# Performance work log

Hardware: AMD Instinct MI355X
Metric: run time of the kernel (lower is better)

## Reference

```python
import jax, jax.numpy as jnp
import numpy as np

N, D, DFF, E, F, K, H = 4096, 512, 512, 512, 4096, 1024, 4


def _rn(i, shape, s=0.02):
    return jax.random.normal(jax.random.fold_in(jax.random.key(0), i), shape, dtype=jnp.float32) * s


def setup_inputs():
    inp = {"inputs": jax.random.normal(jax.random.key(1), (N, D), dtype=jnp.float32)}
    i = 10
    for p in ("enc", "dec"):
        for nm, shp in (("wq", (D, D)), ("wk", (D, D)), ("wv", (D, D)), ("wo", (D, D)), ("w1", (D, DFF)), ("w2", (DFF, D))):
            inp[p + "_" + nm] = _rn(i, shp); i += 1
        for nm, shp in (("bq", (D,)), ("bk", (D,)), ("bv", (D,)), ("bo", (D,)), ("b1", (DFF,)), ("b2", (D,))):
            inp[p + "_" + nm] = jnp.zeros(shp, jnp.float32)
        inp[p + "_ln1_g"] = jnp.ones((D,), jnp.float32)
        inp[p + "_ln1_b"] = jnp.zeros((D,), jnp.float32)
        inp[p + "_ln2_g"] = jnp.ones((D,), jnp.float32)
        inp[p + "_ln2_b"] = jnp.zeros((D,), jnp.float32)
    inp["fc1_w"] = _rn(100, (D, E))
    inp["fc1_b"] = jnp.zeros((E,), jnp.float32)
    inp["fc2_w"] = _rn(101, (D, F))
    inp["fc2_b"] = jnp.zeros((F,), jnp.float32)
    inp["emb"] = _rn(102, (K, E), s=0.01)
    return inp


def layer_norm(x, g, b, eps=1e-6):
    mu = jnp.mean(x, axis=-1, keepdims=True)
    var = jnp.mean(jnp.square(x - mu), axis=-1, keepdims=True)
    return (x - mu) * jax.lax.rsqrt(var + eps) * g + b


def row_distance(a, b):
    # cosine similarity between rows (sim in [-1,1]; loss maps (sim+1)/2 -> [0,1])
    an = a * jax.lax.rsqrt(jnp.maximum(jnp.sum(a * a, axis=1, keepdims=True), 1e-12))
    bn = b * jax.lax.rsqrt(jnp.maximum(jnp.sum(b * b, axis=1, keepdims=True), 1e-12))
    return an @ bn.T


def nearest_context(feature, context):
    distances = row_distance(feature, context) * -1.0  # [N, K]
    min_ind = jnp.argmin(distances, axis=1)
    one_hot = jax.nn.one_hot(min_ind, context.shape[0], dtype=jnp.float32)  # [N, K]
    rslt = one_hot @ jax.lax.stop_gradient(context)  # [N, E]
    return rslt, one_hot


@jax.custom_vjp
def vq(feature, context):
    return nearest_context(feature, context)[0]


def _vq_fwd(feature, context):
    value, ind = nearest_context(feature, context)
    return value, ind


def _vq_bwd(ind, d_value):
    # straight-through to feature, scatter-add (via one-hot matmul) to codebook
    return d_value, ind.T @ d_value


vq.defvjp(_vq_fwd, _vq_bwd)


def encoder_layer(x, wq, bq, wk, bk, wv, bv, wo, bo, w1, b1, w2, b2, g1, be1, g2, be2):
    n, d = x.shape
    dh = d // H
    q = (x @ wq + bq).reshape(n, H, dh)
    k = (x @ wk + bk).reshape(n, H, dh)
    v = (x @ wv + bv).reshape(n, H, dh)
    scores = jnp.einsum('nhd,mhd->hnm', q, k) / jnp.sqrt(jnp.float32(dh))
    attn = jax.nn.softmax(scores, axis=-1)
    ctx = jnp.einsum('hnm,mhd->nhd', attn, v).reshape(n, d)
    out1 = layer_norm(x + (ctx @ wo + bo), g1, be1)
    ffn = jax.nn.relu(out1 @ w1 + b1) @ w2 + b2
    return layer_norm(out1 + ffn, g2, be2)


def reference(inputs, enc_wq, enc_wk, enc_wv, enc_wo, enc_w1, enc_w2, enc_bq, enc_bk, enc_bv, enc_bo, enc_b1, enc_b2, enc_ln1_g, enc_ln1_b, enc_ln2_g, enc_ln2_b, dec_wq, dec_wk, dec_wv, dec_wo, dec_w1, dec_w2, dec_bq, dec_bk, dec_bv, dec_bo, dec_b1, dec_b2, dec_ln1_g, dec_ln1_b, dec_ln2_g, dec_ln2_b, fc1_w, fc1_b, fc2_w, fc2_b, emb):
    encoded = encoder_layer(inputs, enc_wq, enc_bq, enc_wk, enc_bk, enc_wv, enc_bv, enc_wo, enc_bo, enc_w1, enc_b1, enc_w2, enc_b2, enc_ln1_g, enc_ln1_b, enc_ln2_g, enc_ln2_b)
    encoded = encoded @ fc1_w + fc1_b  # [N, E]
    vq_feat = vq(encoded, emb)
    _, context_ind = nearest_context(encoded, emb)
    decoded = encoder_layer(vq_feat, dec_wq, dec_bq, dec_wk, dec_bk, dec_wv, dec_bv, dec_wo, dec_bo, dec_w1, dec_b1, dec_w2, dec_b2, dec_ln1_g, dec_ln1_b, dec_ln2_g, dec_ln2_b)
    decoded = jax.nn.relu(decoded @ fc2_w + fc2_b)  # [N, F]
    return encoded, vq_feat, context_ind, decoded, emb
```

## Files before the change

kernel.cpp:

```cpp
#include <hip/hip_runtime.h>
#include <hip/hip_bf16.h>
#include <stdint.h>

typedef __bf16 bf16;
typedef __bf16 bf16x8 __attribute__((ext_vector_type(8)));
typedef float  f32x4v __attribute__((ext_vector_type(4)));

__device__ __forceinline__ void cvt8(const float* v, bf16x8& hh, bf16x8& ll) {
    #pragma unroll
    for (int j = 0; j < 8; j++) {
        bf16 b = (bf16)v[j]; hh[j] = b; ll[j] = (bf16)(v[j] - (float)b);
    }
}

__device__ __forceinline__ float block_reduce_sum256(float v) {
    __shared__ float red[256];
    int tid = threadIdx.x;
    red[tid] = v; __syncthreads();
    #pragma unroll
    for (int s = 128; s > 0; s >>= 1) {
        if (tid < s) red[tid] += red[tid + s];
        __syncthreads();
    }
    float r = red[0]; __syncthreads();
    return r;
}

template<int BMT, bool RELU, bool TRANS, bool BNAT, bool HILO>
__global__ __launch_bounds__(256, 2)
void gemm3(const float* __restrict__ A, const float* __restrict__ B,
           const float* __restrict__ bias, float* __restrict__ C,
           bf16* __restrict__ Chi, bf16* __restrict__ Clo,
           int K, int lda, int ldb, int ldc, float alpha)
{
    constexpr int BN = 128, TK = 32;
    constexpr int RM = BMT / 32;
    __shared__ __align__(16) bf16 Ah[BMT * TK];
    __shared__ __align__(16) bf16 Al[BMT * TK];
    __shared__ __align__(16) bf16 Bh[BN * TK];
    __shared__ __align__(16) bf16 Bl[BN * TK];

    const int tid  = threadIdx.x;
    const int wave = tid >> 6, lane = tid & 63;
    const int wr = wave >> 1, wc = wave & 1;
    const long bm = (long)blockIdx.y * BMT;
    const long bn = (long)blockIdx.x * BN;
    const int fr = lane & 15, fq = lane >> 4;

    f32x4v acc[RM][4] = {};

    for (int k0 = 0; k0 < K; k0 += TK) {
        #pragma unroll
        for (int it = 0; it < BMT / 64; it++) {
            const int c = it * 256 + tid;
            const int r = c >> 2, k8 = c & 3;
            const float* src = A + (bm + r) * (long)lda + k0 + k8 * 8;
            float4 f0 = ((const float4*)src)[0], f1 = ((const float4*)src)[1];
            float v[8] = {f0.x, f0.y, f0.z, f0.w, f1.x, f1.y, f1.z, f1.w};
            bf16x8 hh, ll; cvt8(v, hh, ll);
            *(bf16x8*)&Ah[r * TK + k8 * 8] = hh;
            *(bf16x8*)&Al[r * TK + k8 * 8] = ll;
        }
        if (BNAT) {
            const int col = tid & 127, bkh = (tid >> 7) * 16;
            const float* src = B + (long)(k0 + bkh) * ldb + bn + col;
            float v[16];
            #pragma unroll
            for (int kk = 0; kk < 16; kk++) v[kk] = src[(long)kk * ldb];
            bf16x8 h0, l0, h1, l1; cvt8(v, h0, l0); cvt8(v + 8, h1, l1);
            bf16* hd = &Bh[col * TK + bkh];
            bf16* ld_ = &Bl[col * TK + bkh];
            ((bf16x8*)hd)[0] = h0; ((bf16x8*)hd)[1] = h1;
            ((bf16x8*)ld_)[0] = l0; ((bf16x8*)ld_)[1] = l1;
        } else {
            #pragma unroll
            for (int it = 0; it < 2; it++) {
                const int c = it * 256 + tid;
                const int r = c >> 2, k8 = c & 3;
                const float* src = B + (bn + r) * (long)ldb + k0 + k8 * 8;
                float4 f0 = ((const float4*)src)[0], f1 = ((const float4*)src)[1];
                float v[8] = {f0.x, f0.y, f0.z, f0.w, f1.x, f1.y, f1.z, f1.w};
                bf16x8 hh, ll; cvt8(v, hh, ll);
                *(bf16x8*)&Bh[r * TK + k8 * 8] = hh;
                *(bf16x8*)&Bl[r * TK + k8 * 8] = ll;
            }
        }
        __syncthreads();

        bf16x8 ah[RM], am[RM], bh[4], bm_[4];
        #pragma unroll
        for (int i = 0; i < RM; i++) {
            const int r = (wr * (BMT / 2) + i * 16 + fr) * TK + fq * 8;
            ah[i] = *(const bf16x8*)&Ah[r];
            am[i] = *(const bf16x8*)&Al[r];
        }
        #pragma unroll
        for (int j = 0; j < 4; j++) {
            const int r = (wc * 64 + j * 16 + fr) * TK + fq * 8;
            bh[j] = *(const bf16x8*)&Bh[r];
            bm_[j] = *(const bf16x8*)&Bl[r];
        }
        #pragma unroll
        for (int i = 0; i < RM; i++)
            #pragma unroll
            for (int j = 0; j < 4; j++) {
                acc[i][j] = __builtin_amdgcn_mfma_f32_16x16x32_bf16(am[i], bh[j], acc[i][j], 0, 0, 0);
                acc[i][j] = __builtin_amdgcn_mfma_f32_16x16x32_bf16(ah[i], bm_[j], acc[i][j], 0, 0, 0);
                acc[i][j] = __builtin_amdgcn_mfma_f32_16x16x32_bf16(ah[i], bh[j], acc[i][j], 0, 0, 0);
            }
        __syncthreads();
    }

    #pragma unroll
    for (int i = 0; i < RM; i++) {
        #pragma unroll
        for (int j = 0; j < 4; j++) {
            const long col = bn + wc * 64 + j * 16 + fr;
            const float bv = bias ? bias[col] : 0.f;
            #pragma unroll
            for (int r = 0; r < 4; r++) {
                const long row = bm + wr * (BMT / 2) + i * 16 + fq * 4 + r;
                float v = acc[i][j][r] * alpha + bv;
                if (RELU) v = fmaxf(v, 0.f);
                const long idx = TRANS ? (col * (long)ldc + row) : (row * (long)ldc + col);
                if (HILO) {
                    bf16 hh = (bf16)v;
                    Chi[idx] = hh;
                    Clo[idx] = (bf16)(v - (float)hh);
                } else {
                    C[idx] = v;
                }
            }
        }
    }
}

__global__ __launch_bounds__(256, 2)
void qkv_gemm(const float* __restrict__ X,
              const float* __restrict__ Wq, const float* __restrict__ Wk, const float* __restrict__ Wv,
              const float* __restrict__ Bq, const float* __restrict__ Bk, const float* __restrict__ Bv,
              float* __restrict__ Qo, bf16* __restrict__ Khi, bf16* __restrict__ Klo,
              bf16* __restrict__ Vthi, bf16* __restrict__ Vtlo)
{
    constexpr int TK = 32, D = 512, N = 4096;
    __shared__ __align__(16) bf16 Ah[64 * TK];
    __shared__ __align__(16) bf16 Al[64 * TK];
    __shared__ __align__(16) bf16 Bh[128 * TK];
    __shared__ __align__(16) bf16 Bl[128 * TK];

    const int tid  = threadIdx.x;
    const int wave = tid >> 6, lane = tid & 63;
    const int wr = wave >> 1, wc = wave & 1;
    const int sel = blockIdx.x >> 2, wcol0 = (blockIdx.x & 3) * 128;
    const long bm = (long)blockIdx.y * 64;
    const int fr = lane & 15, fq = lane >> 4;

    const float* W  = sel == 0 ? Wq : (sel == 1 ? Wk : Wv);
    const float* Bb = sel == 0 ? Bq : (sel == 1 ? Bk : Bv);

    f32x4v acc[2][4] = {};

    for (int k0 = 0; k0 < D; k0 += TK) {
        {
            const int r = tid >> 2, k8 = tid & 3;
            const float* src = X + (bm + r) * (long)D + k0 + k8 * 8;
            float4 f0 = ((const float4*)src)[0], f1 = ((const float4*)src)[1];
            float v[8] = {f0.x, f0.y, f0.z, f0.w, f1.x, f1.y, f1.z, f1.w};
            bf16x8 hh, ll; cvt8(v, hh, ll);
            *(bf16x8*)&Ah[r * TK + k8 * 8] = hh;
            *(bf16x8*)&Al[r * TK + k8 * 8] = ll;
        }
        {
            const int col = tid & 127, bkh = (tid >> 7) * 16;
            const float* src = W + (long)(k0 + bkh) * D + wcol0 + col;
            float v[16];
            #pragma unroll
            for (int kk = 0; kk < 16; kk++) v[kk] = src[(long)kk * D];
            bf16x8 h0, l0, h1, l1; cvt8(v, h0, l0); cvt8(v + 8, h1, l1);
            bf16* hd = &Bh[col * TK + bkh];
            bf16* ld_ = &Bl[col * TK + bkh];
            ((bf16x8*)hd)[0] = h0; ((bf16x8*)hd)[1] = h1;
            ((bf16x8*)ld_)[0] = l0; ((bf16x8*)ld_)[1] = l1;
        }
        __syncthreads();

        bf16x8 ah[2], am[2], bh[4], bm_[4];
        #pragma unroll
        for (int i = 0; i < 2; i++) {
            const int r = (wr * 32 + i * 16 + fr) * TK + fq * 8;
            ah[i] = *(const bf16x8*)&Ah[r];
            am[i] = *(const bf16x8*)&Al[r];
        }
        #pragma unroll
        for (int j = 0; j < 4; j++) {
            const int r = (wc * 64 + j * 16 + fr) * TK + fq * 8;
            bh[j] = *(const bf16x8*)&Bh[r];
            bm_[j] = *(const bf16x8*)&Bl[r];
        }
        #pragma unroll
        for (int i = 0; i < 2; i++)
            #pragma unroll
            for (int j = 0; j < 4; j++) {
                acc[i][j] = __builtin_amdgcn_mfma_f32_16x16x32_bf16(am[i], bh[j], acc[i][j], 0, 0, 0);
                acc[i][j] = __builtin_amdgcn_mfma_f32_16x16x32_bf16(ah[i], bm_[j], acc[i][j], 0, 0, 0);
                acc[i][j] = __builtin_amdgcn_mfma_f32_16x16x32_bf16(ah[i], bh[j], acc[i][j], 0, 0, 0);
            }
        __syncthreads();
    }

    #pragma unroll
    for (int i = 0; i < 2; i++) {
        #pragma unroll
        for (int j = 0; j < 4; j++) {
            const int col = wc * 64 + j * 16 + fr;
            const float bv = Bb[wcol0 + col];
            #pragma unroll
            for (int r = 0; r < 4; r++) {
                const long row = bm + wr * 32 + i * 16 + fq * 4 + r;
                const float v = acc[i][j][r] + bv;
                if (sel == 0) {
                    Qo[row * D + wcol0 + col] = v;
                } else {
                    const bf16 hh = (bf16)v;
                    const bf16 ll = (bf16)(v - (float)hh);
                    const long idx = (sel == 1) ? (row * (long)D + wcol0 + col)
                                                : ((long)(wcol0 + col) * N + row);
                    if (sel == 1) { Khi[idx] = hh; Klo[idx] = ll; }
                    else          { Vthi[idx] = hh; Vtlo[idx] = ll; }
                }
            }
        }
    }
}

__global__ __launch_bounds__(128, 2)
void flash_attn(const float* __restrict__ Q,
                const bf16* __restrict__ Khi, const bf16* __restrict__ Klo,
                const bf16* __restrict__ Vthi, const bf16* __restrict__ Vtlo,
                float* __restrict__ Op, float* __restrict__ ml)
{
    constexpr int N = 4096, D = 512, SPAN = 1024, TKV = 32, NT = SPAN / TKV;
    constexpr float TS = 0.12751791f;

    __shared__ __align__(16) bf16 smem[16384];
    bf16* Kh = smem;
    bf16* Kl = smem + 4096;
    bf16* Vh = smem + 8192;
    bf16* Vl = smem + 12288;

    const int tid = threadIdx.x;
    const int wave = tid >> 6, lane = tid & 63;
    const int fr = lane & 15, fq = lane >> 4;
    const int qt = blockIdx.x, h = blockIdx.y, s = blockIdx.z;
    const long q0 = (long)qt * 64;

    const int kn = tid >> 4, kk8 = tid & 15;
    const int vd = tid >> 2, vk8 = tid & 3;

    bf16x8 qh[2][4], ql[2][4];
    #pragma unroll
    for (int rg = 0; rg < 2; rg++)
        #pragma unroll
        for (int kt = 0; kt < 4; kt++) {
            const float* src = Q + (q0 + wave * 32 + rg * 16 + fr) * D + h * 128 + kt * 32 + fq * 8;
            float4 f0 = ((const float4*)src)[0], f1 = ((const float4*)src)[1];
            float v[8] = {f0.x, f0.y, f0.z, f0.w, f1.x, f1.y, f1.z, f1.w};
            cvt8(v, qh[rg][kt], ql[rg][kt]);
        }

    f32x4v o[2][8] = {};
    float m_run[2] = {-1e30f, -1e30f}, l_run[2] = {0.f, 0.f};

    const int j0base = s * SPAN;

    #pragma unroll 1
    for (int jt = 0; jt < NT; jt++) {
        const int j0 = j0base + jt * TKV;

        #pragma unroll
        for (int i = 0; i < 4; i++) {
            const int n = kn + 8 * i;
            const long kg = (long)(j0 + n) * D + h * 128 + kk8 * 8;
            const int ko = n * 128 + ((kk8 ^ (n & 15)) << 3);
            *(uint4*)&Kh[ko] = *(const uint4*)&Khi[kg];
            *(uint4*)&Kl[ko] = *(const uint4*)&Klo[kg];
            const int d = vd + 32 * i;
            const long vg = (long)(h * 128 + d) * N + j0 + vk8 * 8;
            const int vo = d * 32 + ((vk8 ^ ((d >> 2) & 3)) << 3);
            *(uint4*)&Vh[vo] = *(const uint4*)&Vthi[vg];
            *(uint4*)&Vl[vo] = *(const uint4*)&Vtlo[vg];
        }
        __syncthreads();

        f32x4v sacc[2][2] = {};
        #pragma unroll
        for (int jb = 0; jb < 2; jb++) {
            bf16x8 kh[4], km[4];
            #pragma unroll
            for (int kt = 0; kt < 4; kt++) {
                const int off = (jb * 16 + fr) * 128 + (((kt * 4 + fq) ^ fr) << 3);
                kh[kt] = *(const bf16x8*)&Kh[off];
                km[kt] = *(const bf16x8*)&Kl[off];
            }
            __builtin_amdgcn_s_setprio(1);
            #pragma unroll
            for (int kt = 0; kt < 4; kt++)
                #pragma unroll
                for (int rg = 0; rg < 2; rg++) {
                    sacc[rg][jb] = __builtin_amdgcn_mfma_f32_16x16x32_bf16(km[kt], qh[rg][kt], sacc[rg][jb], 0, 0, 0);
                    sacc[rg][jb] = __builtin_amdgcn_mfma_f32_16x16x32_bf16(kh[kt], ql[rg][kt], sacc[rg][jb], 0, 0, 0);
                    sacc[rg][jb] = __builtin_amdgcn_mfma_f32_16x16x32_bf16(kh[kt], qh[rg][kt], sacc[rg][jb], 0, 0, 0);
                }
            __builtin_amdgcn_s_setprio(0);
        }

        bf16x8 ph[2], pl[2];
        float alpha[2];
        #pragma unroll
        for (int rg = 0; rg < 2; rg++) {
            float t[2][4];
            float mloc = -1e30f;
            #pragma unroll
            for (int jb = 0; jb < 2; jb++)
                #pragma unroll
                for (int r = 0; r < 4; r++) {
                    t[jb][r] = sacc[rg][jb][r] * TS;
                    mloc = fmaxf(mloc, t[jb][r]);
                }
            mloc = fmaxf(mloc, __shfl_xor(mloc, 16));
            mloc = fmaxf(mloc, __shfl_xor(mloc, 32));
            const float mn = fmaxf(m_run[rg], mloc);
            alpha[rg] = exp2f(m_run[rg] - mn);
            m_run[rg] = mn;

            float p[2][4];
            float rs = 0.f;
            #pragma unroll
            for (int jb = 0; jb < 2; jb++)
                #pragma unroll
                for (int r = 0; r < 4; r++) {
                    p[jb][r] = exp2f(t[jb][r] - mn);
                    rs += p[jb][r];
                }
            rs += __shfl_xor(rs, 16);
            rs += __shfl_xor(rs, 32);
            l_run[rg] = l_run[rg] * alpha[rg] + rs;

            unsigned int hp[2][2], lp[2][2];
            #pragma unroll
            for (int jb = 0; jb < 2; jb++)
                #pragma unroll
                for (int t2 = 0; t2 < 2; t2++) {
                    const float p0 = p[jb][2 * t2], p1 = p[jb][2 * t2 + 1];
                    const bf16 h0 = (bf16)p0, h1 = (bf16)p1;
                    const unsigned short u0 = __builtin_bit_cast(unsigned short, h0);
                    const unsigned short u1 = __builtin_bit_cast(unsigned short, h1);
                    hp[jb][t2] = (unsigned int)u0 | ((unsigned int)u1 << 16);
                    const bf16 g0 = (bf16)(p0 - (float)h0), g1 = (bf16)(p1 - (float)h1);
                    const unsigned short w0 = __builtin_bit_cast(unsigned short, g0);
                    const unsigned short w1 = __builtin_bit_cast(unsigned short, g1);
                    lp[jb][t2] = (unsigned int)w0 | ((unsigned int)w1 << 16);
                }

            uint4 PH, PL;
            {
                unsigned int phw[4], plw[4];
                #pragma unroll
                for (int w = 0; w < 4; w++) {
                    const int src = ((2 * (fq & 1) + (w >> 1)) << 4) + fr;
                    const unsigned int h0 = (unsigned int)__shfl((int)hp[0][w & 1], src);
                    const unsigned int h1 = (unsigned int)__shfl((int)hp[1][w & 1], src);
                    phw[w] = (fq >> 1) ? h1 : h0;
                    const unsigned int g0 = (unsigned int)__shfl((int)lp[0][w & 1], src);
                    const unsigned int g1 = (unsigned int)__shfl((int)lp[1][w & 1], src);
                    plw[w] = (fq >> 1) ? g1 : g0;
                }
                PH.x = phw[0]; PH.y = phw[1]; PH.z = phw[2]; PH.w = phw[3];
                PL.x = plw[0]; PL.y = plw[1]; PL.z = plw[2]; PL.w = plw[3];
            }
            ph[rg] = __builtin_bit_cast(bf16x8, PH);
            pl[rg] = __builtin_bit_cast(bf16x8, PL);
        }

        #pragma unroll
        for (int rg = 0; rg < 2; rg++) {
            float alr[4];
            #pragma unroll
            for (int r = 0; r < 4; r++) alr[r] = __shfl(alpha[rg], fq * 4 + r);
            #pragma unroll
            for (int jbo = 0; jbo < 8; jbo++)
                #pragma unroll
                for (int r = 0; r < 4; r++)
                    o[rg][jbo][r] *= alr[r];
        }

        #pragma unroll
        for (int jbo = 0; jbo < 8; jbo++) {
            const int off = (jbo * 16 + fr) * 32 + ((fq ^ ((fr >> 2) & 3)) << 3);
            const bf16x8 vh_ = *(const bf16x8*)&Vh[off];
            const bf16x8 vl_ = *(const bf16x8*)&Vl[off];
            __builtin_amdgcn_s_setprio(1);
            #pragma unroll
            for (int rg = 0; rg < 2; rg++) {
                o[rg][jbo] = __builtin_amdgcn_mfma_f32_16x16x32_bf16(pl[rg], vh_, o[rg][jbo], 0, 0, 0);
                o[rg][jbo] = __builtin_amdgcn_mfma_f32_16x16x32_bf16(ph[rg], vl_, o[rg][jbo], 0, 0, 0);
                o[rg][jbo] = __builtin_amdgcn_mfma_f32_16x16x32_bf16(ph[rg], vh_, o[rg][jbo], 0, 0, 0);
            }
            __builtin_amdgcn_s_setprio(0);
        }
        __syncthreads();
    }

    const long sidx = (long)((h * 64 + qt) * 4 + s);
    float* ob = Op + sidx * 8192;
    #pragma unroll
    for (int rg = 0; rg < 2; rg++)
        #pragma unroll
        for (int jbo = 0; jbo < 8; jbo++)
            #pragma unroll
            for (int r = 0; r < 4; r++) {
                const int lrow = wave * 32 + rg * 16 + fq * 4 + r;
                ob[lrow * 128 + jbo * 16 + fr] = o[rg][jbo][r];
            }
    if (fq == 0) {
        #pragma unroll
        for (int rg = 0; rg < 2; rg++) {
            const int lrow = wave * 32 + rg * 16 + fr;
            ml[sidx * 128 + lrow]      = m_run[rg];
            ml[sidx * 128 + 64 + lrow] = l_run[rg];
        }
    }
}

__global__ void flash_merge(const float* __restrict__ Op, const float* __restrict__ ml,
                            float* __restrict__ ctx)
{
    const int idx = blockIdx.x;
    const int h = idx >> 6, qt = idx & 63;
    const int tid = threadIdx.x;
    __shared__ float es[4][64], il[64];
    if (tid < 64) {
        float m[4], l[4];
        #pragma unroll
        for (int s = 0; s < 4; s++) {
            m[s] = ml[(long)(idx * 4 + s) * 128 + tid];
            l[s] = ml[(long)(idx * 4 + s) * 128 + 64 + tid];
        }
        float mx = fmaxf(fmaxf(m[0], m[1]), fmaxf(m[2], m[3]));
        float denom = 0.f;
        #pragma unroll
        for (int s = 0; s < 4; s++) {
            const float e = exp2f(m[s] - mx);
            es[s][tid] = e;
            denom += e * l[s];
        }
        il[tid] = 1.f / denom;
    }
    __syncthreads();
    const long b = (long)idx * 4 * 8192;
    #pragma unroll
    for (int i = 0; i < 32; i++) {
        const int e = tid + i * 256;
        const int row = e >> 7, col = e & 127;
        float v = es[0][row] * Op[b + e] + es[1][row] * Op[b + 8192 + e]
                + es[2][row] * Op[b + 16384 + e] + es[3][row] * Op[b + 24576 + e];
        ctx[(long)(qt * 64 + row) * 512 + h * 128 + col] = v * il[row];
    }
}

__global__ void add_ln_f32(const float* __restrict__ a, const float* __restrict__ b,
                           const float* __restrict__ g, const float* __restrict__ be,
                           float* __restrict__ out)
{
    const long row = blockIdx.x;
    const int tid = threadIdx.x;
    const long base = row * 512L;
    float x0 = a[base + tid]       + b[base + tid];
    float x1 = a[base + tid + 256] + b[base + tid + 256];
    float s = block_reduce_sum256(x0 + x1);
    float mu = s * (1.f / 512.f);
    float d0 = x0 - mu, d1 = x1 - mu;
    float var = block_reduce_sum256(d0 * d0 + d1 * d1) * (1.f / 512.f);
    float invs = rsqrtf(var + 1e-6f);
    out[base + tid]       = d0 * invs * g[tid]       + be[tid];
    out[base + tid + 256] = d1 * invs * g[tid + 256] + be[tid + 256];
}

__global__ void normalize_emb(const float* __restrict__ emb, float* __restrict__ embn)
{
    const long row = blockIdx.x;
    const int tid = threadIdx.x;
    const long base = row * 512L;
    float a0 = emb[base + tid];
    float a1 = emb[base + tid + 256];
    float ss = block_reduce_sum256(a0 * a0 + a1 * a1);
    float sc = rsqrtf(fmaxf(ss, 1e-12f));
    embn[base + tid]       = a0 * sc;
    embn[base + tid + 256] = a1 * sc;
}

__global__ void vq_select_onehot(float* __restrict__ sims, const float* __restrict__ emb,
                                 float* __restrict__ vq_out)
{
    __shared__ float sv[256];
    __shared__ int   si[256];
    const long row = blockIdx.x;
    const int tid = threadIdx.x;
    float* s = sims + row * 1024L;
    float v0 = s[tid], v1 = s[tid + 256], v2 = s[tid + 512], v3 = s[tid + 768];
    float best = v0; int bi = tid;
    if (v1 > best) { best = v1; bi = tid + 256; }
    if (v2 > best) { best = v2; bi = tid + 512; }
    if (v3 > best) { best = v3; bi = tid + 768; }
    sv[tid] = best; si[tid] = bi; __syncthreads();
    #pragma unroll
    for (int st = 128; st > 0; st >>= 1) {
        if (tid < st) {
            if (sv[tid + st] > sv[tid] ||
                (sv[tid + st] == sv[tid] && si[tid + st] < si[tid])) {
                sv[tid] = sv[tid + st]; si[tid] = si[tid + st];
            }
        }
        __syncthreads();
    }
    const int idx = si[0];
    s[tid]       = (tid       == idx) ? 1.f : 0.f;
    s[tid + 256] = (tid + 256 == idx) ? 1.f : 0.f;
    s[tid + 512] = (tid + 512 == idx) ? 1.f : 0.f;
    s[tid + 768] = (tid + 768 == idx) ? 1.f : 0.f;
    const float* er = emb + (long)idx * 512;
    float* vr = vq_out + row * 512L;
    vr[tid]       = er[tid];
    vr[tid + 256] = er[tid + 256];
}

struct EncW {
    const float *wq, *wk, *wv, *wo, *w1, *w2;
    const float *bq, *bk, *bv, *bo, *b1, *b2;
    const float *g1, *be1, *g2, *be2;
};

static void run_encoder_g3(hipStream_t stream, const float* x, const EncW& w,
                           float* qb, bf16* khi, bf16* klo, bf16* vthi, bf16* vtlo,
                           float* ctx, float* Op, float* ml,
                           float* x1, float* hb, float* out)
{
    const int N = 4096, D = 512;
    qkv_gemm<<<dim3(12, 64), 256, 0, stream>>>(
        x, w.wq, w.wk, w.wv, w.bq, w.bk, w.bv, qb, khi, klo, vthi, vtlo);
    flash_attn<<<dim3(64, 4, 4), 128, 0, stream>>>(qb, khi, klo, vthi, vtlo, Op, ml);
    flash_merge<<<256, 256, 0, stream>>>(Op, ml, ctx);
    gemm3<64, false, false, true, false><<<dim3(4, 64), 256, 0, stream>>>(
        ctx, w.wo, w.bo, qb, nullptr, nullptr, D, D, D, D, 1.f);
    add_ln_f32<<<N, 256, 0, stream>>>(x, qb, w.g1, w.be1, x1);
    gemm3<64, true, false, true, false><<<dim3(4, 64), 256, 0, stream>>>(
        x1, w.w1, w.b1, hb, nullptr, nullptr, D, D, D, D, 1.f);
    gemm3<64, false, false, true, false><<<dim3(4, 64), 256, 0, stream>>>(
        hb, w.w2, w.b2, qb, nullptr, nullptr, D, D, D, D, 1.f);
    add_ln_f32<<<N, 256, 0, stream>>>(x1, qb, w.g2, w.be2, out);
}

extern "C" void kernel_launch(void* const* d_in, const int* in_sizes, int n_in,
                              void* d_out, int out_size, void* d_ws, size_t ws_size,
                              hipStream_t stream)
{
    const int N = 4096, D = 512, E = 512, F = 4096, KCB = 1024;
    (void)in_sizes; (void)n_in; (void)out_size; (void)d_ws; (void)ws_size;

    const float* x_in  = (const float*)d_in[0];
    const float* fc1_w = (const float*)d_in[33];
    const float* fc1_b = (const float*)d_in[34];
    const float* fc2_w = (const float*)d_in[35];
    const float* fc2_b = (const float*)d_in[36];
    const float* emb   = (const float*)d_in[37];

    float* out0 = (float*)d_out;
    float* out1 = out0 + (size_t)N * E;
    float* out2 = out1 + (size_t)N * E;
    float* out3 = out2 + (size_t)N * KCB;
    float* out4 = out3 + (size_t)N * F;

    char* arena = (char*)out3;
    const size_t MB = 1024 * 1024;
    float* qb     = (float*)(arena + 0 * MB);
    bf16*  khi    = (bf16*) (arena + 8 * MB);
    bf16*  klo    = (bf16*) (arena + 12 * MB);
    bf16*  vthi   = (bf16*) (arena + 16 * MB);
    bf16*  vtlo   = (bf16*) (arena + 20 * MB);
    float* ctx    = (float*)(arena + 24 * MB);
    float* Op     = (float*)(arena + 32 * MB);
    float* decout = (float*)(arena + 56 * MB);
    float* x1     = (float*)(arena + 16 * MB);
    float* hb     = (float*)(arena + 8 * MB);
    float* ml     = (float*)out4;
    float* embn   = out1;
    float* stage  = (float*)out4;

    EncW ew = { (const float*)d_in[1],  (const float*)d_in[2],  (const float*)d_in[3],
                (const float*)d_in[4],  (const float*)d_in[5],  (const float*)d_in[6],
                (const float*)d_in[7],  (const float*)d_in[8],  (const float*)d_in[9],
                (const float*)d_in[10], (const float*)d_in[11], (const float*)d_in[12],
                (const float*)d_in[13], (const float*)d_in[14], (const float*)d_in[15],
                (const float*)d_in[16] };
    EncW dw = { (const float*)d_in[17], (const float*)d_in[18], (const float*)d_in[19],
                (const float*)d_in[20], (const float*)d_in[21], (const float*)d_in[22],
                (const float*)d_in[23], (const float*)d_in[24], (const float*)d_in[25],
                (const float*)d_in[26], (const float*)d_in[27], (const float*)d_in[28],
                (const float*)d_in[29], (const float*)d_in[30], (const float*)d_in[31],
                (const float*)d_in[32] };

    normalize_emb<<<KCB, 256, 0, stream>>>(emb, embn);
    run_encoder_g3(stream, x_in, ew, qb, khi, klo, vthi, vtlo, ctx, Op, ml, x1, hb, ctx);

    gemm3<64, false, false, true, false><<<dim3(4, 64), 256, 0, stream>>>(
        ctx, fc1_w, fc1_b, out0, nullptr, nullptr, D, D, E, E, 1.f);

    gemm3<128, false, false, false, false><<<dim3(8, 32), 256, 0, stream>>>(
        out0, embn, nullptr, out2, nullptr, nullptr, E, E, E, KCB, 1.f);
    vq_select_onehot<<<N, 256, 0, stream>>>(out2, emb, out1);

    run_encoder_g3(stream, out1, dw, qb, khi, klo, vthi, vtlo, ctx, Op, ml, x1, hb, decout);

    hipMemcpyAsync(stage, decout + (size_t)3584 * D, (size_t)512 * D * sizeof(float),
                   hipMemcpyDeviceToDevice, stream);
    gemm3<128, true, false, true, false><<<dim3(F / 128, 3584 / 128), 256, 0, stream>>>(
        decout, fc2_w, fc2_b, out3, nullptr, nullptr, D, D, F, F, 1.f);
    gemm3<128, true, false, true, false><<<dim3(F / 128, 512 / 128), 256, 0, stream>>>(
        stage, fc2_w, fc2_b, out3 + (size_t)3584 * F, nullptr, nullptr, D, D, F, F, 1.f);

    hipMemcpyAsync(out4, emb, (size_t)KCB * E * sizeof(float), hipMemcpyDeviceToDevice, stream);
}
```

Before: 897.0 us.

## Pre-split weights into transposed bf16 hi/lo once and use packed GEMMs

```diff
diff --git a/kernel.cpp b/kernel.cpp
--- a/kernel.cpp
+++ b/kernel.cpp
@@ -130,6 +130,92 @@
                 } else {
                     C[idx] = v;
                 }
+            }
+        }
+    }
+}
+
+template<int BMT, bool RELU>
+__global__ __launch_bounds__(256, 2)
+void gemm3p(const float* __restrict__ A,
+            const bf16* __restrict__ Bph, const bf16* __restrict__ Bpl,
+            const float* __restrict__ bias, float* __restrict__ C,
+            int K, int lda, int ldb, int ldc)
+{
+    constexpr int BN = 128, TK = 32;
+    constexpr int RM = BMT / 32;
+    __shared__ __align__(16) bf16 Ah[BMT * TK];
+    __shared__ __align__(16) bf16 Al[BMT * TK];
+    __shared__ __align__(16) bf16 Bh[BN * TK];
+    __shared__ __align__(16) bf16 Bl[BN * TK];
+
+    const int tid  = threadIdx.x;
+    const int wave = tid >> 6, lane = tid & 63;
+    const int wr = wave >> 1, wc = wave & 1;
+    const long bm = (long)blockIdx.y * BMT;
+    const long bn = (long)blockIdx.x * BN;
+    const int fr = lane & 15, fq = lane >> 4;
+
+    f32x4v acc[RM][4] = {};
+
+    for (int k0 = 0; k0 < K; k0 += TK) {
+        #pragma unroll
+        for (int it = 0; it < BMT / 64; it++) {
+            const int c = it * 256 + tid;
+            const int r = c >> 2, k8 = c & 3;
+            const float* src = A + (bm + r) * (long)lda + k0 + k8 * 8;
+            float4 f0 = ((const float4*)src)[0], f1 = ((const float4*)src)[1];
+            float v[8] = {f0.x, f0.y, f0.z, f0.w, f1.x, f1.y, f1.z, f1.w};
+            bf16x8 hh, ll; cvt8(v, hh, ll);
+            *(bf16x8*)&Ah[r * TK + k8 * 8] = hh;
+            *(bf16x8*)&Al[r * TK + k8 * 8] = ll;
+        }
+        #pragma unroll
+        for (int it = 0; it < 2; it++) {
+            const int c = it * 256 + tid;
+            const int r = c >> 2, k8 = c & 3;
+            const long bo = (bn + r) * (long)ldb + k0 + k8 * 8;
+            *(uint4*)&Bh[r * TK + k8 * 8] = *(const uint4*)&Bph[bo];
+            *(uint4*)&Bl[r * TK + k8 * 8] = *(const uint4*)&Bpl[bo];
+        }
+        __syncthreads();
+
+        bf16x8 ah[RM], am[RM], bh[4], bm_[4];
+        #pragma unroll
+        for (int i = 0; i < RM; i++) {
+            const int r = (wr * (BMT / 2) + i * 16 + fr) * TK + fq * 8;
+            ah[i] = *(const bf16x8*)&Ah[r];
+            am[i] = *(const bf16x8*)&Al[r];
+        }
+        #pragma unroll
+        for (int j = 0; j < 4; j++) {
+            const int r = (wc * 64 + j * 16 + fr) * TK + fq * 8;
+            bh[j] = *(const bf16x8*)&Bh[r];
+            bm_[j] = *(const bf16x8*)&Bl[r];
+        }
+        #pragma unroll
+        for (int i = 0; i < RM; i++)
+            #pragma unroll
+            for (int j = 0; j < 4; j++) {
+                acc[i][j] = __builtin_amdgcn_mfma_f32_16x16x32_bf16(am[i], bh[j], acc[i][j], 0, 0, 0);
+                acc[i][j] = __builtin_amdgcn_mfma_f32_16x16x32_bf16(ah[i], bm_[j], acc[i][j], 0, 0, 0);
+                acc[i][j] = __builtin_amdgcn_mfma_f32_16x16x32_bf16(ah[i], bh[j], acc[i][j], 0, 0, 0);
+            }
+        __syncthreads();
+    }
+
+    #pragma unroll
+    for (int i = 0; i < RM; i++) {
+        #pragma unroll
+        for (int j = 0; j < 4; j++) {
+            const long col = bn + wc * 64 + j * 16 + fr;
+            const float bv = bias ? bias[col] : 0.f;
+            #pragma unroll
+            for (int r = 0; r < 4; r++) {
+                const long row = bm + wr * (BMT / 2) + i * 16 + fq * 4 + r;
+                float v = acc[i][j][r] + bv;
+                if (RELU) v = fmaxf(v, 0.f);
+                C[row * (long)ldc + col] = v;
             }
         }
     }
@@ -230,6 +316,139 @@
                 }
             }
         }
+    }
+}
+
+__global__ __launch_bounds__(256, 2)
+void qkv_gemmp(const float* __restrict__ X,
+               const bf16* __restrict__ Wqh, const bf16* __restrict__ Wql,
+               const bf16* __restrict__ Wkh, const bf16* __restrict__ Wkl,
+               const bf16* __restrict__ Wvh, const bf16* __restrict__ Wvl,
+               const float* __restrict__ Bq, const float* __restrict__ Bk, const float* __restrict__ Bv,
+               float* __restrict__ Qo, bf16* __restrict__ Khi, bf16* __restrict__ Klo,
+               bf16* __restrict__ Vthi, bf16* __restrict__ Vtlo)
+{
+    constexpr int TK = 32, D = 512, N = 4096;
+    __shared__ __align__(16) bf16 Ah[64 * TK];
+    __shared__ __align__(16) bf16 Al[64 * TK];
+    __shared__ __align__(16) bf16 Bh[128 * TK];
+    __shared__ __align__(16) bf16 Bl[128 * TK];
+
+    const int tid  = threadIdx.x;
+    const int wave = tid >> 6, lane = tid & 63;
+    const int wr = wave >> 1, wc = wave & 1;
+    const int sel = blockIdx.x >> 2, wcol0 = (blockIdx.x & 3) * 128;
+    const long bm = (long)blockIdx.y * 64;
+    const int fr = lane & 15, fq = lane >> 4;
+
+    const bf16* Wh = sel == 0 ? Wqh : (sel == 1 ? Wkh : Wvh);
+    const bf16* Wl = sel == 0 ? Wql : (sel == 1 ? Wkl : Wvl);
+    const float* Bb = sel == 0 ? Bq : (sel == 1 ? Bk : Bv);
+
+    f32x4v acc[2][4] = {};
+
+    for (int k0 = 0; k0 < D; k0 += TK) {
+        {
+            const int r = tid >> 2, k8 = tid & 3;
+            const float* src = X + (bm + r) * (long)D + k0 + k8 * 8;
+            float4 f0 = ((const float4*)src)[0], f1 = ((const float4*)src)[1];
+            float v[8] = {f0.x, f0.y, f0.z, f0.w, f1.x, f1.y, f1.z, f1.w};
+            bf16x8 hh, ll; cvt8(v, hh, ll);
+            *(bf16x8*)&Ah[r * TK + k8 * 8] = hh;
+            *(bf16x8*)&Al[r * TK + k8 * 8] = ll;
+        }
+        #pragma unroll
+        for (int it = 0; it < 2; it++) {
+            const int c = it * 256 + tid;
+            const int r = c >> 2, k8 = c & 3;
+            const long bo = (long)(wcol0 + r) * D + k0 + k8 * 8;
+            *(uint4*)&Bh[r * TK + k8 * 8] = *(const uint4*)&Wh[bo];
+            *(uint4*)&Bl[r * TK + k8 * 8] = *(const uint4*)&Wl[bo];
+        }
+        __syncthreads();
+
+        bf16x8 ah[2], am[2], bh[4], bm_[4];
+        #pragma unroll
+        for (int i = 0; i < 2; i++) {
+            const int r = (wr * 32 + i * 16 + fr) * TK + fq * 8;
+            ah[i] = *(const bf16x8*)&Ah[r];
+            am[i] = *(const bf16x8*)&Al[r];
+        }
+        #pragma unroll
+        for (int j = 0; j < 4; j++) {
+            const int r = (wc * 64 + j * 16 + fr) * TK + fq * 8;
+            bh[j] = *(const bf16x8*)&Bh[r];
+            bm_[j] = *(const bf16x8*)&Bl[r];
+        }
+        #pragma unroll
+        for (int i = 0; i < 2; i++)
+            #pragma unroll
+            for (int j = 0; j < 4; j++) {
+                acc[i][j] = __builtin_amdgcn_mfma_f32_16x16x32_bf16(am[i], bh[j], acc[i][j], 0, 0, 0);
+                acc[i][j] = __builtin_amdgcn_mfma_f32_16x16x32_bf16(ah[i], bm_[j], acc[i][j], 0, 0, 0);
+                acc[i][j] = __builtin_amdgcn_mfma_f32_16x16x32_bf16(ah[i], bh[j], acc[i][j], 0, 0, 0);
+            }
+        __syncthreads();
+    }
+
+    #pragma unroll
+    for (int i = 0; i < 2; i++) {
+        #pragma unroll
+        for (int j = 0; j < 4; j++) {
+            const int col = wc * 64 + j * 16 + fr;
+            const float bv = Bb[wcol0 + col];
+            #pragma unroll
+            for (int r = 0; r < 4; r++) {
+                const long row = bm + wr * 32 + i * 16 + fq * 4 + r;
+                const float v = acc[i][j][r] + bv;
+                if (sel == 0) {
+                    Qo[row * D + wcol0 + col] = v;
+                } else {
+                    const bf16 hh = (bf16)v;
+                    const bf16 ll = (bf16)(v - (float)hh);
+                    const long idx = (sel == 1) ? (row * (long)D + wcol0 + col)
+                                                : ((long)(wcol0 + col) * N + row);
+                    if (sel == 1) { Khi[idx] = hh; Klo[idx] = ll; }
+                    else          { Vthi[idx] = hh; Vtlo[idx] = ll; }
+                }
+            }
+        }
+    }
+}
+
+struct W14 { const float* w[14]; };
+
+__global__ void convert_weights(W14 p, bf16* __restrict__ wsb)
+{
+    const int z = blockIdx.z;
+    const int tid = threadIdx.x;
+    int wi, n0, N_;
+    if (z < 13) { wi = z; n0 = blockIdx.y * 32; N_ = 512; }
+    else        { wi = 13; n0 = (z - 13) * 512 + blockIdx.y * 32; N_ = 4096; }
+    const int k0 = blockIdx.x * 32;
+    const float* W = p.w[wi];
+    const long base = (wi < 13) ? (long)wi * 524288 : 6815744L;
+    const long hsz  = (wi < 13) ? 262144L : 2097152L;
+    bf16* hi = wsb + base;
+    bf16* lo = wsb + base + hsz;
+
+    __shared__ float tile[32][33];
+    #pragma unroll
+    for (int i = 0; i < 4; i++) {
+        const int idx = i * 256 + tid;
+        const int r = idx >> 5, c = idx & 31;
+        tile[r][c] = W[(long)(k0 + r) * N_ + n0 + c];
+    }
+    __syncthreads();
+    #pragma unroll
+    for (int i = 0; i < 4; i++) {
+        const int idx = i * 256 + tid;
+        const int r = idx >> 5, c = idx & 31;
+        const float v = tile[c][r];
+        const bf16 h = (bf16)v;
+        const long o = (long)(n0 + r) * 512 + k0 + c;
+        hi[o] = h;
+        lo[o] = (bf16)(v - (float)h);
     }
 }
 
@@ -499,6 +718,24 @@
     embn[base + tid + 256] = a1 * sc;
 }
 
+__global__ void normalize_emb_p(const float* __restrict__ emb,
+                                bf16* __restrict__ hi, bf16* __restrict__ lo)
+{
+    const long row = blockIdx.x;
+    const int tid = threadIdx.x;
+    const long base = row * 512L;
+    float a0 = emb[base + tid];
+    float a1 = emb[base + tid + 256];
+    float ss = block_reduce_sum256(a0 * a0 + a1 * a1);
+    float sc = rsqrtf(fmaxf(ss, 1e-12f));
+    const float e0 = a0 * sc, e1 = a1 * sc;
+    const bf16 h0 = (bf16)e0, h1 = (bf16)e1;
+    hi[base + tid]       = h0;
+    lo[base + tid]       = (bf16)(e0 - (float)h0);
+    hi[base + tid + 256] = h1;
+    lo[base + tid + 256] = (bf16)(e1 - (float)h1);
+}
+
 __global__ void vq_select_onehot(float* __restrict__ sims, const float* __restrict__ emb,
                                  float* __restrict__ vq_out)
 {
@@ -560,12 +797,36 @@
     add_ln_f32<<<N, 256, 0, stream>>>(x1, qb, w.g2, w.be2, out);
 }
 
+static void run_encoder_g3p(hipStream_t stream, const float* x, const EncW& w,
+                            bf16* wsb, int slot0,
+                            float* qb, bf16* khi, bf16* klo, bf16* vthi, bf16* vtlo,
+                            float* ctx, float* Op, float* ml,
+                            float* x1, float* hb, float* out)
+{
+    const int N = 4096, D = 512;
+    auto sh = [&](int i) { return wsb + (long)(slot0 + i) * 524288; };
+    auto sl = [&](int i) { return wsb + (long)(slot0 + i) * 524288 + 262144; };
+    qkv_gemmp<<<dim3(12, 64), 256, 0, stream>>>(
+        x, sh(0), sl(0), sh(1), sl(1), sh(2), sl(2),
+        w.bq, w.bk, w.bv, qb, khi, klo, vthi, vtlo);
+    flash_attn<<<dim3(64, 4, 4), 128, 0, stream>>>(qb, khi, klo, vthi, vtlo, Op, ml);
+    flash_merge<<<256, 256, 0, stream>>>(Op, ml, ctx);
+    gemm3p<64, false><<<dim3(4, 64), 256, 0, stream>>>(
+        ctx, sh(3), sl(3), w.bo, qb, D, D, D, D);
+    add_ln_f32<<<N, 256, 0, stream>>>(x, qb, w.g1, w.be1, x1);
+    gemm3p<64, true><<<dim3(4, 64), 256, 0, stream>>>(
+        x1, sh(4), sl(4), w.b1, hb, D, D, D, D);
+    gemm3p<64, false><<<dim3(4, 64), 256, 0, stream>>>(
+        hb, sh(5), sl(5), w.b2, qb, D, D, D, D);
+    add_ln_f32<<<N, 256, 0, stream>>>(x1, qb, w.g2, w.be2, out);
+}
+
 extern "C" void kernel_launch(void* const* d_in, const int* in_sizes, int n_in,
                               void* d_out, int out_size, void* d_ws, size_t ws_size,
                               hipStream_t stream)
 {
     const int N = 4096, D = 512, E = 512, F = 4096, KCB = 1024;
-    (void)in_sizes; (void)n_in; (void)out_size; (void)d_ws; (void)ws_size;
+    (void)in_sizes; (void)n_in; (void)out_size;
 
     const float* x_in  = (const float*)d_in[0];
     const float* fc1_w = (const float*)d_in[33];
@@ -609,24 +870,57 @@
                 (const float*)d_in[29], (const float*)d_in[30], (const float*)d_in[31],
                 (const float*)d_in[32] };
 
-    normalize_emb<<<KCB, 256, 0, stream>>>(emb, embn);
-    run_encoder_g3(stream, x_in, ew, qb, khi, klo, vthi, vtlo, ctx, Op, ml, x1, hb, ctx);
-
-    gemm3<64, false, false, true, false><<<dim3(4, 64), 256, 0, stream>>>(
-        ctx, fc1_w, fc1_b, out0, nullptr, nullptr, D, D, E, E, 1.f);
-
-    gemm3<128, false, false, false, false><<<dim3(8, 32), 256, 0, stream>>>(
-        out0, embn, nullptr, out2, nullptr, nullptr, E, E, E, KCB, 1.f);
-    vq_select_onehot<<<N, 256, 0, stream>>>(out2, emb, out1);
-
-    run_encoder_g3(stream, out1, dw, qb, khi, klo, vthi, vtlo, ctx, Op, ml, x1, hb, decout);
-
-    hipMemcpyAsync(stage, decout + (size_t)3584 * D, (size_t)512 * D * sizeof(float),
-                   hipMemcpyDeviceToDevice, stream);
-    gemm3<128, true, false, true, false><<<dim3(F / 128, 3584 / 128), 256, 0, stream>>>(
-        decout, fc2_w, fc2_b, out3, nullptr, nullptr, D, D, F, F, 1.f);
-    gemm3<128, true, false, true, false><<<dim3(F / 128, 512 / 128), 256, 0, stream>>>(
-        stage, fc2_w, fc2_b, out3 + (size_t)3584 * F, nullptr, nullptr, D, D, F, F, 1.f);
-
-    hipMemcpyAsync(out4, emb, (size_t)KCB * E * sizeof(float), hipMemcpyDeviceToDevice, stream);
-}
+    const size_t WS_NEED = 24117248;
+    const bool pre = (d_ws != nullptr) && (ws_size >= WS_NEED);
+
+    if (pre) {
+        bf16* wsb = (bf16*)d_ws;
+        bf16* f2h = wsb + 6815744;  bf16* f2l = f2h + 2097152;
+        bf16* enh = wsb + 11010048; bf16* enl = enh + 524288;
+
+        W14 ptrs;
+        ptrs.w[0]  = ew.wq; ptrs.w[1]  = ew.wk; ptrs.w[2]  = ew.wv;
+        ptrs.w[3]  = ew.wo; ptrs.w[4]  = ew.w1; ptrs.w[5]  = ew.w2;
+        ptrs.w[6]  = dw.wq; ptrs.w[7]  = dw.wk; ptrs.w[8]  = dw.wv;
+        ptrs.w[9]  = dw.wo; ptrs.w[10] = dw.w1; ptrs.w[11] = dw.w2;
+        ptrs.w[12] = fc1_w; ptrs.w[13] = fc2_w;
+        convert_weights<<<dim3(16, 16, 21), 256, 0, stream>>>(ptrs, wsb);
+        normalize_emb_p<<<KCB, 256, 0, stream>>>(emb, enh, enl);
+
+        run_encoder_g3p(stream, x_in, ew, wsb, 0, qb, khi, klo, vthi, vtlo, ctx, Op, ml, x1, hb, ctx);
+
+        gemm3p<64, false><<<dim3(4, 64), 256, 0, stream>>>(
+            ctx, wsb + 12L * 524288, wsb + 12L * 524288 + 262144, fc1_b, out0, D, D, D, E);
+
+        gemm3p<128, false><<<dim3(8, 32), 256, 0, stream>>>(
+            out0, enh, enl, nullptr, out2, E, E, E, KCB);
+        vq_select_onehot<<<N, 256, 0, stream>>>(out2, emb, out1);
+
+        run_encoder_g3p(stream, out1, dw, wsb, 6, qb, khi, klo, vthi, vtlo, ctx, Op, ml, x1, hb, decout);
+
+        hipMemcpyAsync(stage, decout + (size_t)3584 * D, (size_t)512 * D * sizeof(float),
+                       hipMemcpyDeviceToDevice, stream);
+        gemm3p<128, true><<<dim3(F / 128, 3584 / 128), 256, 0, stream>>>(
+            decout, f2h, f2l, fc2_b, out3, D, D, D, F);
+        gemm3p<128, true><<<dim3(F / 128, 512 / 128), 256, 0, stream>>>(
+            stage, f2h, f2l, fc2_b, out3 + (size_t)3584 * F, D, D, D, F);
+
+        hipMemcpyAsync(out4, emb, (size_t)KCB * E * sizeof(float), hipMemcpyDeviceToDevice, stream);
+    } else {
+        normalize_emb<<<KCB, 256, 0, stream>>>(emb, embn);
+        run_encoder_g3(stream, x_in, ew, qb, khi, klo, vthi, vtlo, ctx, Op, ml, x1, hb, ctx);
+        gemm3<64, false, false, true, false><<<dim3(4, 64), 256, 0, stream>>>(
+            ctx, fc1_w, fc1_b, out0, nullptr, nullptr, D, D, E, E, 1.f);
+        gemm3<128, false, false, false, false><<<dim3(8, 32), 256, 0, stream>>>(
+            out0, embn, nullptr, out2, nullptr, nullptr, E, E, E, KCB, 1.f);
+        vq_select_onehot<<<N, 256, 0, stream>>>(out2, emb, out1);
+        run_encoder_g3(stream, out1, dw, qb, khi, klo, vthi, vtlo, ctx, Op, ml, x1, hb, decout);
+        hipMemcpyAsync(stage, decout + (size_t)3584 * D, (size_t)512 * D * sizeof(float),
+                       hipMemcpyDeviceToDevice, stream);
+        gemm3<128, true, false, true, false><<<dim3(F / 128, 3584 / 128), 256, 0, stream>>>(
+            decout, fc2_w, fc2_b, out3, nullptr, nullptr, D, D, F, F, 1.f);
+        gemm3<128, true, false, true, false><<<dim3(F / 128, 512 / 128), 256, 0, stream>>>(
+            stage, fc2_w, fc2_b, out3 + (size_t)3584 * F, nullptr, nullptr, D, D, F, F, 1.f);
+        hipMemcpyAsync(out4, emb, (size_t)KCB * E * sizeof(float), hipMemcpyDeviceToDevice, stream);
+    }
+}
```

After: 822.0 us. 1.09x faster.
